# Kernel tuning notes

Hardware: AMD Instinct MI355X
Metric: run time of the kernel (lower is better)

## Reference

```python
import jax, jax.numpy as jnp
import numpy as np

N, E = 50000, 800000
F_IN, E_DIM, D, H = 128, 64, 64, 4  # per-head channels D, heads H; concat=False -> out dim D
GROUPS = 16
EPS = 1e-5


def _p(key, shape, scale):
    return (jax.random.normal(key, shape, dtype=jnp.float32) * scale)


def setup_inputs() -> dict:
    key = jax.random.key(0)
    ks = jax.random.split(key, 40)
    inp = {
        "x": jax.random.normal(ks[0], (N, F_IN), dtype=jnp.float32),
        "edge_index": jax.random.randint(ks[1], (2, E), 0, N, dtype=jnp.int64),
        "edge_attr": jax.random.normal(ks[2], (E, E_DIM), dtype=jnp.float32),
    }
    # TransformerConv params, layer i: Wq/Wk/Wv [in, H*D] (+bias), We [E_DIM, H*D] (no bias),
    # Wskip [in, D] (+bias).  Layer 1 in=F_IN, layers 2/3 in=D.
    idx = 3
    for i, fin in zip((1, 2, 3), (F_IN, D, D)):
        s = 1.0 / np.sqrt(fin)
        se = 1.0 / np.sqrt(E_DIM)
        inp[f"Wq{i}"] = _p(ks[idx + 0], (fin, H * D), s)
        inp[f"bq{i}"] = jnp.zeros((H * D,), jnp.float32)
        inp[f"Wk{i}"] = _p(ks[idx + 1], (fin, H * D), s)
        inp[f"bk{i}"] = jnp.zeros((H * D,), jnp.float32)
        inp[f"Wv{i}"] = _p(ks[idx + 2], (fin, H * D), s)
        inp[f"bv{i}"] = jnp.zeros((H * D,), jnp.float32)
        inp[f"We{i}"] = _p(ks[idx + 3], (E_DIM, H * D), se)
        inp[f"Wskip{i}"] = _p(ks[idx + 4], (fin, D), s)
        inp[f"bskip{i}"] = jnp.zeros((D,), jnp.float32)
        idx += 5
    inp["gn_w"] = jnp.ones((D,), jnp.float32)
    inp["gn_b"] = jnp.zeros((D,), jnp.float32)
    return inp


def transformer_conv(x, src, dst, edge_attr, Wq, bq, Wk, bk, Wv, bv, We, Wskip, bskip):
    n = x.shape[0]
    q = (x @ Wq + bq).reshape(n, H, D)
    k = (x @ Wk + bk).reshape(n, H, D)
    v = (x @ Wv + bv).reshape(n, H, D)
    e = (edge_attr @ We).reshape(-1, H, D)  # [E,H,D]
    k_e = k[src] + e                          # edge-level key
    v_e = v[src] + e                          # edge-level value
    alpha = jnp.einsum('ehd,ehd->eh', q[dst], k_e) / np.sqrt(D)  # [E,H]
    # segment softmax over incoming edges of each dst node
    amax = jax.ops.segment_max(alpha, dst, num_segments=n)
    amax = jnp.where(jnp.isfinite(amax), amax, 0.0)
    ex = jnp.exp(alpha - amax[dst])
    denom = jax.ops.segment_sum(ex, dst, num_segments=n)
    attn = ex / (denom[dst] + 1e-16)
    out = jax.ops.segment_sum(attn[:, :, None] * v_e, dst, num_segments=n)  # [N,H,D]
    out = out.mean(axis=1)                     # concat=False -> mean over heads
    return out + (x @ Wskip + bskip)           # root_weight skip


def group_norm(x, w, b):
    n, c = x.shape
    xg = x.reshape(n, GROUPS, c // GROUPS)
    mu = xg.mean(axis=2, keepdims=True)
    var = xg.var(axis=2, keepdims=True)
    xn = ((xg - mu) * jax.lax.rsqrt(var + EPS)).reshape(n, c)
    return xn * w + b


def reference(x, edge_index, edge_attr,
              Wq1, bq1, Wk1, bk1, Wv1, bv1, We1, Wskip1, bskip1,
              Wq2, bq2, Wk2, bk2, Wv2, bv2, We2, Wskip2, bskip2,
              Wq3, bq3, Wk3, bk3, Wv3, bv3, We3, Wskip3, bskip3,
              gn_w, gn_b):
    src, dst = edge_index[0], edge_index[1]
    layers = [
        (Wq1, bq1, Wk1, bk1, Wv1, bv1, We1, Wskip1, bskip1),
        (Wq2, bq2, Wk2, bk2, Wv2, bv2, We2, Wskip2, bskip2),
        (Wq3, bq3, Wk3, bk3, Wv3, bv3, We3, Wskip3, bskip3),
    ]
    h = x
    for prm in layers:
        h = transformer_conv(h, src, dst, edge_attr, *prm)
        h = group_norm(h, gn_w, gn_b)
        h = jax.nn.gelu(h, approximate=False)
    return h
```

## Files before the change

kernel.cpp:

```cpp
#include <hip/hip_runtime.h>
#include <math.h>

#define NN 50000
#define NE 800000
#define NCOLS 1088

typedef long long i64;
typedef unsigned short u16;
typedef short bf16x8 __attribute__((ext_vector_type(8)));
typedef unsigned short u16x8 __attribute__((ext_vector_type(8)));
typedef float f32x4 __attribute__((ext_vector_type(4)));

static __device__ __forceinline__ float bf2f(u16 u) {
  union { float f; unsigned b; } x; x.b = ((unsigned)u) << 16; return x.f;
}
static __device__ __forceinline__ u16 f2bf(float f) {
  union { float f; unsigned b; } x; x.f = f;
  unsigned r = x.b + 0x7FFFu + ((x.b >> 16) & 1u);
  return (u16)(r >> 16);
}

__global__ void detect_i64(const int* __restrict__ ei32, int* __restrict__ flag) {
  int i = blockIdx.x * blockDim.x + threadIdx.x;
  if (i < 2048) {
    if (ei32[2 * i + 1] != 0) atomicOr(flag, 1);
  }
}

__global__ void extract_edges(const void* __restrict__ ei, const int* __restrict__ flag,
                              int* __restrict__ src32, int* __restrict__ dst32, int ne) {
  int is32 = *flag;
  int i = blockIdx.x * blockDim.x + threadIdx.x;
  int st = gridDim.x * blockDim.x;
  if (is32) {
    const int* p = (const int*)ei;
    for (; i < ne; i += st) { src32[i] = p[i]; dst32[i] = p[ne + i]; }
  } else {
    const i64* p = (const i64*)ei;
    for (; i < ne; i += st) { src32[i] = (int)p[i]; dst32[i] = (int)p[ne + i]; }
  }
}

__global__ void hist_kernel(const int* __restrict__ dst, int* __restrict__ deg, int ne) {
  int i = blockIdx.x * blockDim.x + threadIdx.x;
  int st = gridDim.x * blockDim.x;
  for (; i < ne; i += st) atomicAdd(&deg[dst[i]], 1);
}

#define SCHUNK 1024
__global__ void scanA(const int* __restrict__ deg, int* __restrict__ row_ptr,
                      int* __restrict__ csum, int n) {
  __shared__ int buf[SCHUNK];
  int c = blockIdx.x, t = threadIdx.x;
  int idx = c * SCHUNK + t;
  int v = (idx < n) ? deg[idx] : 0;
  buf[t] = v;
  __syncthreads();
  for (int off = 1; off < SCHUNK; off <<= 1) {
    int x = (t >= off) ? buf[t - off] : 0;
    __syncthreads();
    buf[t] += x;
    __syncthreads();
  }
  if (idx < n) row_ptr[idx + 1] = buf[t];
  if (t == SCHUNK - 1) csum[c] = buf[t];
}

__global__ void scanB(int* __restrict__ csum, int nchunks) {
  if (threadIdx.x == 0 && blockIdx.x == 0) {
    int run = 0;
    for (int c = 0; c < nchunks; ++c) { int v = csum[c]; csum[c] = run; run += v; }
  }
}

__global__ void scanC(int* __restrict__ row_ptr, const int* __restrict__ csum, int n) {
  int c = blockIdx.x, t = threadIdx.x;
  int idx = c * SCHUNK + t;
  if (idx < n) row_ptr[idx + 1] += csum[c];
  if (idx == 0) row_ptr[0] = 0;
}

__global__ void scatter_kernel(const int* __restrict__ src, const int* __restrict__ dst,
                               const int* __restrict__ row_ptr, int* __restrict__ cursor,
                               int* __restrict__ src_sorted, int* __restrict__ eid_sorted, int ne) {
  int i = blockIdx.x * blockDim.x + threadIdx.x;
  int st = gridDim.x * blockDim.x;
  for (; i < ne; i += st) {
    int d = dst[i];
    int pos = row_ptr[d] + atomicAdd(&cursor[d], 1);
    src_sorted[pos] = src[i];
    eid_sorted[pos] = i;
  }
}

__global__ void sort_lists(const int* __restrict__ row_ptr, int* __restrict__ src_sorted,
                           int* __restrict__ eid_sorted, int n) {
  int node = blockIdx.x * blockDim.x + threadIdx.x;
  if (node >= n) return;
  int beg = row_ptr[node], end = row_ptr[node + 1];
  for (int a = beg + 1; a < end; ++a) {
    int e = eid_sorted[a], s = src_sorted[a];
    int b = a - 1;
    while (b >= beg && eid_sorted[b] > e) {
      eid_sorted[b + 1] = eid_sorted[b];
      src_sorted[b + 1] = src_sorted[b];
      --b;
    }
    eid_sorted[b + 1] = e; src_sorted[b + 1] = s;
  }
}

__global__ void ea_gather(const int* __restrict__ eid_sorted, const float* __restrict__ ea,
                          float* __restrict__ ea_csr, int ne) {
  long total = (long)ne * 16;
  long st = (long)gridDim.x * blockDim.x;
  for (long i = (long)blockIdx.x * blockDim.x + threadIdx.x; i < total; i += st) {
    int j = (int)(i >> 4);
    int c = (int)(i & 15);
    int e = eid_sorted[j];
    ((float4*)ea_csr)[i] = ((const float4*)ea)[(size_t)e * 16 + c];
  }
}

__global__ void cvt_split(const float* __restrict__ in, u16* __restrict__ hi,
                          u16* __restrict__ lo, int nElem) {
  int i = blockIdx.x * blockDim.x + threadIdx.x;
  int st = gridDim.x * blockDim.x;
  for (; i < nElem; i += st) {
    float v = in[i];
    u16 h = f2bf(v);
    hi[i] = h;
    lo[i] = f2bf(v - bf2f(h));
  }
}

__global__ void prep_wt(const float* __restrict__ Wq, const float* __restrict__ Wk,
                        const float* __restrict__ Wv, const float* __restrict__ We,
                        const float* __restrict__ Wsk, float* __restrict__ Wt, int fin) {
  int i = blockIdx.x * blockDim.x + threadIdx.x;
  if (i >= NCOLS * fin) return;
  int col = i / fin, k = i % fin;
  float val;
  if (col < 768) {
    const float* W = (col < 256) ? Wq : (col < 512) ? Wk : Wv;
    val = W[k * 256 + (col & 255)];
  } else if (col < 1024) {
    int idx = col - 768; int h = idx >> 6, ce = idx & 63;
    float a = 0.f;
    for (int d = 0; d < 64; ++d) a += Wq[k * 256 + h * 64 + d] * We[ce * 256 + h * 64 + d];
    val = a;
  } else {
    val = Wsk[k * 64 + (col - 1024)];
  }
  Wt[(size_t)col * fin + k] = val;
}

__global__ void prep_bias(const float* __restrict__ bq, const float* __restrict__ bk,
                          const float* __restrict__ bv, const float* __restrict__ We,
                          const float* __restrict__ bsk, float* __restrict__ bb) {
  int col = blockIdx.x * blockDim.x + threadIdx.x;
  if (col >= NCOLS) return;
  float val;
  if (col < 768) {
    const float* b = (col < 256) ? bq : (col < 512) ? bk : bv;
    val = b[col & 255];
  } else if (col < 1024) {
    int idx = col - 768; int h = idx >> 6, ce = idx & 63;
    float a = 0.f;
    for (int d = 0; d < 64; ++d) a += bq[h * 64 + d] * We[ce * 256 + h * 64 + d];
    val = a;
  } else {
    val = bsk[col - 1024];
  }
  bb[col] = val;
}

__global__ void prep_wpost(const float* __restrict__ We, float* __restrict__ Wt2) {
  int i = blockIdx.x * blockDim.x + threadIdx.x;
  if (i >= 64 * 256) return;
  int col = i >> 8, k = i & 255;
  int h = k >> 6, ce = k & 63;
  Wt2[i] = We[ce * 256 + h * 64 + col];
}

__global__ __launch_bounds__(256) void node_gemm_mfma(
    const u16* __restrict__ Xhi, const u16* __restrict__ Xlo,
    const u16* __restrict__ Whi, const u16* __restrict__ Wlo,
    const float* __restrict__ bb,
    float* __restrict__ qq_tab, float* __restrict__ kv_tab,
    float* __restrict__ skip_tab, int n, int fin) {
  __shared__ __align__(16) u16 Ah[64][72];
  __shared__ __align__(16) u16 Al[64][72];
  __shared__ __align__(16) u16 Bh[64][72];
  __shared__ __align__(16) u16 Bl[64][72];
  int tid = threadIdx.x, wave = tid >> 6, lane = tid & 63;
  int c0 = blockIdx.x * 64, m0 = blockIdx.y * 64;
  f32x4 acc[4];
  #pragma unroll
  for (int i = 0; i < 4; ++i) acc[i] = (f32x4){0.f, 0.f, 0.f, 0.f};

  int lr = tid >> 2, sg = (tid & 3) * 16;
  for (int k0 = 0; k0 < fin; k0 += 64) {
    u16x8 z = {0, 0, 0, 0, 0, 0, 0, 0};
    u16x8 a0 = z, a1 = z, l0 = z, l1 = z;
    if (m0 + lr < n) {
      const u16* ph = &Xhi[(size_t)(m0 + lr) * fin + k0 + sg];
      a0 = *(const u16x8*)ph; a1 = *(const u16x8*)(ph + 8);
      const u16* pl = &Xlo[(size_t)(m0 + lr) * fin + k0 + sg];
      l0 = *(const u16x8*)pl; l1 = *(const u16x8*)(pl + 8);
    }
    *(u16x8*)&Ah[lr][sg] = a0; *(u16x8*)&Ah[lr][sg + 8] = a1;
    *(u16x8*)&Al[lr][sg] = l0; *(u16x8*)&Al[lr][sg + 8] = l1;
    {
      const u16* ph = &Whi[(size_t)(c0 + lr) * fin + k0 + sg];
      *(u16x8*)&Bh[lr][sg] = *(const u16x8*)ph;
      *(u16x8*)&Bh[lr][sg + 8] = *(const u16x8*)(ph + 8);
      const u16* pl = &Wlo[(size_t)(c0 + lr) * fin + k0 + sg];
      *(u16x8*)&Bl[lr][sg] = *(const u16x8*)pl;
      *(u16x8*)&Bl[lr][sg + 8] = *(const u16x8*)(pl + 8);
    }
    __syncthreads();
    int arow = wave * 16 + (lane & 15);
    int kb = (lane >> 4) * 8;
    #pragma unroll
    for (int ks = 0; ks < 2; ++ks) {
      bf16x8 ah = *(const bf16x8*)&Ah[arow][ks * 32 + kb];
      bf16x8 al_ = *(const bf16x8*)&Al[arow][ks * 32 + kb];
      #pragma unroll
      for (int nf = 0; nf < 4; ++nf) {
        bf16x8 bh = *(const bf16x8*)&Bh[nf * 16 + (lane & 15)][ks * 32 + kb];
        bf16x8 bl = *(const bf16x8*)&Bl[nf * 16 + (lane & 15)][ks * 32 + kb];
        acc[nf] = __builtin_amdgcn_mfma_f32_16x16x32_bf16(ah, bh, acc[nf], 0, 0, 0);
        acc[nf] = __builtin_amdgcn_mfma_f32_16x16x32_bf16(ah, bl, acc[nf], 0, 0, 0);
        acc[nf] = __builtin_amdgcn_mfma_f32_16x16x32_bf16(al_, bh, acc[nf], 0, 0, 0);
      }
    }
    __syncthreads();
  }
  int rbase = m0 + wave * 16 + (lane >> 4) * 4;
  int cl = lane & 15;
  #pragma unroll
  for (int nf = 0; nf < 4; ++nf) {
    int col = c0 + nf * 16 + cl;
    float bias = bb[col];
    #pragma unroll
    for (int r = 0; r < 4; ++r) {
      int row = rbase + r;
      if (row >= n) continue;
      float val = acc[nf][r] + bias;
      if (col < 256)        qq_tab[(size_t)row * 512 + col] = val;
      else if (col < 768)   kv_tab[(size_t)row * 512 + col - 256] = val;
      else if (col < 1024)  qq_tab[(size_t)row * 512 + col - 512] = val;
      else                  skip_tab[(size_t)row * 64 + col - 1024] = val;
    }
  }
}

__global__ __launch_bounds__(256) void attn_kernel_v6(
    const int* __restrict__ row_ptr, const int* __restrict__ src_sorted,
    const int* __restrict__ eid_sorted, const float* __restrict__ ea,
    const float* __restrict__ ea_csr, int use_csr,
    const float* __restrict__ qq_tab, const float* __restrict__ kv_tab,
    float* __restrict__ avs_tab, float* __restrict__ awn_tab, int n) {
  int tid = threadIdx.x;
  int wave = tid >> 6, lane = tid & 63;
  int c16 = lane & 15;
  const float4* qq4 = (const float4*)qq_tab;
  const float4* kv4 = (const float4*)kv_tab;
  const float4* ec4 = (const float4*)ea_csr;
  const float4* e4p = (const float4*)ea;

  int node = blockIdx.x * 4 + wave;
  if (node >= n) return;
  int beg = row_ptr[node];
  int deg = row_ptr[node + 1] - beg;

  float4 q4 = qq4[(size_t)node * 128 + lane];
  float4 t4 = qq4[(size_t)node * 128 + 64 + lane];

  float m = -INFINITY, s = 0.f;
  float4 av = make_float4(0.f, 0.f, 0.f, 0.f);
  float4 aw = make_float4(0.f, 0.f, 0.f, 0.f);

#define LDE(j_, K_, V_, E_)                                   \
  {                                                           \
    int jc = (j_); int jm = beg + deg - 1;                    \
    if (jc > jm) jc = jm;                                     \
    int s_ = src_sorted[jc];                                  \
    const float4* kr = kv4 + (size_t)s_ * 128;                \
    K_ = kr[lane]; V_ = kr[64 + lane];                        \
    if (use_csr) E_ = ec4[(size_t)jc * 16 + c16];             \
    else { int e_ = eid_sorted[jc];                           \
           E_ = e4p[(size_t)e_ * 16 + c16]; }                 \
  }

#define PROC(K_, V_, E_)                                      \
  {                                                           \
    float p = q4.x * K_.x + q4.y * K_.y + q4.z * K_.z + q4.w * K_.w \
            + t4.x * E_.x + t4.y * E_.y + t4.z * E_.z + t4.w * E_.w; \
    p += __shfl_xor(p, 1);                                    \
    p += __shfl_xor(p, 2);                                    \
    p += __shfl_xor(p, 4);                                    \
    p += __shfl_xor(p, 8);                                    \
    p *= 0.125f;                                              \
    float d_ = p - m;                                         \
    float e_ = __expf(-fabsf(d_));                            \
    float sc = d_ > 0.f ? e_ : 1.f;                           \
    float pp = d_ > 0.f ? 1.f : e_;                           \
    m = fmaxf(m, p);                                          \
    s = s * sc + pp;                                          \
    av.x = av.x * sc + pp * V_.x; av.y = av.y * sc + pp * V_.y; \
    av.z = av.z * sc + pp * V_.z; av.w = av.w * sc + pp * V_.w; \
    aw.x = aw.x * sc + pp * E_.x; aw.y = aw.y * sc + pp * E_.y; \
    aw.z = aw.z * sc + pp * E_.z; aw.w = aw.w * sc + pp * E_.w; \
  }

  if (deg > 0) {
    float4 KA, VA, EA, KB, VB, EB;
    LDE(beg + 0, KA, VA, EA);
    LDE(beg + 1, KB, VB, EB);
    int t = 0;
    for (; t + 1 < deg; t += 2) {
      {
        float4 nK, nV, nE;
        LDE(beg + t + 2, nK, nV, nE);
        PROC(KA, VA, EA);
        KA = nK; VA = nV; EA = nE;
      }
      {
        float4 nK, nV, nE;
        LDE(beg + t + 3, nK, nV, nE);
        PROC(KB, VB, EB);
        KB = nK; VB = nV; EB = nE;
      }
    }
    if (t < deg) PROC(KA, VA, EA);
  }

  float inv = s > 0.f ? 1.f / s : 0.f;
  float4 awn = make_float4(aw.x * inv, aw.y * inv, aw.z * inv, aw.w * inv);
  float4 avn = make_float4(av.x * inv, av.y * inv, av.z * inv, av.w * inv);

  ((float4*)awn_tab)[(size_t)node * 64 + lane] = awn;

  avn.x += __shfl_xor(avn.x, 16); avn.y += __shfl_xor(avn.y, 16);
  avn.z += __shfl_xor(avn.z, 16); avn.w += __shfl_xor(avn.w, 16);
  avn.x += __shfl_xor(avn.x, 32); avn.y += __shfl_xor(avn.y, 32);
  avn.z += __shfl_xor(avn.z, 32); avn.w += __shfl_xor(avn.w, 32);
  if (lane < 16)
    ((float4*)avs_tab)[(size_t)node * 16 + c16] = avn;
}

__global__ __launch_bounds__(256) void post_gn(
    const float* __restrict__ A, const float* __restrict__ B,
    const float* __restrict__ avs, const float* __restrict__ skip,
    const float* __restrict__ gnw, const float* __restrict__ gnb,
    float* __restrict__ out_f32, u16* __restrict__ out_hi, u16* __restrict__ out_lo, int n) {
  __shared__ __align__(16) float Xs[128][68];
  __shared__ __align__(16) float Ws[64][68];
  int tid = threadIdx.x;
  int tx = tid & 15, ty = tid >> 4;
  int m0 = blockIdx.x * 128;
  float acc[8][4];
  #pragma unroll
  for (int i = 0; i < 8; ++i)
    #pragma unroll
    for (int j = 0; j < 4; ++j) acc[i][j] = 0.f;

  for (int k0 = 0; k0 < 256; k0 += 64) {
    #pragma unroll
    for (int p = 0; p < 8; ++p) {
      int r = ty + 16 * p;
      float4 xv = make_float4(0.f, 0.f, 0.f, 0.f);
      if (m0 + r < n) xv = *(const float4*)&A[(size_t)(m0 + r) * 256 + k0 + tx * 4];
      *(float4*)&Xs[r][tx * 4] = xv;
    }
    #pragma unroll
    for (int p = 0; p < 4; ++p) {
      int r = ty + 16 * p;
      float4 wv = *(const float4*)&B[(size_t)r * 256 + k0 + tx * 4];
      *(float4*)&Ws[r][tx * 4] = wv;
    }
    __syncthreads();
    #pragma unroll 4
    for (int kk = 0; kk < 64; kk += 4) {
      float4 a[8], b[4];
      #pragma unroll
      for (int i = 0; i < 8; ++i) a[i] = *(const float4*)&Xs[ty + 16 * i][kk];
      #pragma unroll
      for (int j = 0; j < 4; ++j) b[j] = *(const float4*)&Ws[tx + 16 * j][kk];
      #pragma unroll
      for (int i = 0; i < 8; ++i)
        #pragma unroll
        for (int j = 0; j < 4; ++j) {
          acc[i][j] = fmaf(a[i].x, b[j].x, acc[i][j]);
          acc[i][j] = fmaf(a[i].y, b[j].y, acc[i][j]);
          acc[i][j] = fmaf(a[i].z, b[j].z, acc[i][j]);
          acc[i][j] = fmaf(a[i].w, b[j].w, acc[i][j]);
        }
    }
    __syncthreads();
  }
  #pragma unroll
  for (int j = 0; j < 4; ++j)
    #pragma unroll
    for (int i = 0; i < 8; ++i)
      Xs[ty + 16 * i][tx + 16 * j] = acc[i][j];
  __syncthreads();

  #pragma unroll
  for (int rep = 0; rep < 8; ++rep) {
    int id = tid + 256 * rep;
    int rl = id >> 4, grp = id & 15;
    int row = m0 + rl;
    if (row >= n) continue;
    float4 a = ((const float4*)avs)[(size_t)row * 16 + grp];
    float4 sk = ((const float4*)skip)[(size_t)row * 16 + grp];
    float4 gw = ((const float4*)gnw)[grp];
    float4 gb = ((const float4*)gnb)[grp];
    float p0 = Xs[rl][grp * 4 + 0], p1 = Xs[rl][grp * 4 + 1];
    float p2 = Xs[rl][grp * 4 + 2], p3 = Xs[rl][grp * 4 + 3];
    float v0 = 0.25f * (a.x + p0) + sk.x;
    float v1 = 0.25f * (a.y + p1) + sk.y;
    float v2 = 0.25f * (a.z + p2) + sk.z;
    float v3 = 0.25f * (a.w + p3) + sk.w;
    float mu = ((v0 + v1) + (v2 + v3)) * 0.25f;
    float d0 = v0 - mu, d1 = v1 - mu, d2 = v2 - mu, d3 = v3 - mu;
    float var = ((d0 * d0 + d1 * d1) + (d2 * d2 + d3 * d3)) * 0.25f;
    float r = rsqrtf(var + 1e-5f);
    float y0 = d0 * r * gw.x + gb.x;
    float y1 = d1 * r * gw.y + gb.y;
    float y2 = d2 * r * gw.z + gb.z;
    float y3 = d3 * r * gw.w + gb.w;
    #define GELU(y) (0.5f * (y) * (1.0f + erff((y) * 0.70710678118654752f)))
    float g0 = GELU(y0), g1 = GELU(y1), g2 = GELU(y2), g3 = GELU(y3);
    if (out_f32) {
      float4 o; o.x = g0; o.y = g1; o.z = g2; o.w = g3;
      ((float4*)out_f32)[(size_t)row * 16 + grp] = o;
    } else {
      u16 h0 = f2bf(g0), h1 = f2bf(g1), h2 = f2bf(g2), h3 = f2bf(g3);
      ushort4 hv; hv.x = h0; hv.y = h1; hv.z = h2; hv.w = h3;
      *(ushort4*)&out_hi[(size_t)row * 64 + grp * 4] = hv;
      ushort4 lv;
      lv.x = f2bf(g0 - bf2f(h0)); lv.y = f2bf(g1 - bf2f(h1));
      lv.z = f2bf(g2 - bf2f(h2)); lv.w = f2bf(g3 - bf2f(h3));
      *(ushort4*)&out_lo[(size_t)row * 64 + grp * 4] = lv;
    }
  }
}

extern "C" void kernel_launch(void* const* d_in, const int* in_sizes, int n_in,
                              void* d_out, int out_size, void* d_ws, size_t ws_size,
                              hipStream_t stream) {
  (void)in_sizes; (void)n_in;
  const float* x = (const float*)d_in[0];
  const void* ei = d_in[1];
  const float* ea = (const float*)d_in[2];
  const float *Wq[3], *bq[3], *Wk[3], *bk[3], *Wv[3], *bv[3], *We[3], *Wsk[3], *bsk[3];
  for (int L = 0; L < 3; ++L) {
    int b = 3 + 9 * L;
    Wq[L] = (const float*)d_in[b + 0]; bq[L] = (const float*)d_in[b + 1];
    Wk[L] = (const float*)d_in[b + 2]; bk[L] = (const float*)d_in[b + 3];
    Wv[L] = (const float*)d_in[b + 4]; bv[L] = (const float*)d_in[b + 5];
    We[L] = (const float*)d_in[b + 6]; Wsk[L] = (const float*)d_in[b + 7];
    bsk[L] = (const float*)d_in[b + 8];
  }
  const float* gnw = (const float*)d_in[30];
  const float* gnb = (const float*)d_in[31];

  char* p = (char*)d_ws;
  auto alloc = [&](size_t bytes) -> void* {
    void* r = (void*)p;
    p += (bytes + 255) & ~(size_t)255;
    return r;
  };
  float* qq_tab = (float*)alloc((size_t)NN * 512 * 4);
  float* kv_tab = (float*)alloc((size_t)NN * 512 * 4);
  float* skip_tab = (float*)alloc((size_t)NN * 64 * 4);
  float* avs_tab = (float*)alloc((size_t)NN * 64 * 4);
  float* awn_tab = (float*)alloc((size_t)NN * 256 * 4);
  u16* xhi = (u16*)alloc((size_t)NN * 128 * 2);
  u16* xlo = (u16*)alloc((size_t)NN * 128 * 2);
  u16* hhi = (u16*)alloc((size_t)NN * 64 * 2);
  u16* hlo = (u16*)alloc((size_t)NN * 64 * 2);
  int* row_ptr = (int*)alloc((size_t)(NN + 1) * 4);
  int* deg = (int*)alloc((size_t)NN * 4);
  int* cursor = (int*)alloc((size_t)NN * 4);
  int* csum = (int*)alloc(1024 * 4);
  int* src_sorted = (int*)alloc((size_t)NE * 4);
  int* eid_sorted = (int*)alloc((size_t)NE * 4);
  int* src32 = (int*)alloc((size_t)NE * 4);
  int* dst32 = (int*)alloc((size_t)NE * 4);
  int* flag = (int*)alloc(256);
  float* Wt[3]; float* bb[3]; float* Wt2[3];
  u16 *whi[3], *wlo[3];
  Wt[0] = (float*)alloc((size_t)NCOLS * 128 * 4);
  Wt[1] = (float*)alloc((size_t)NCOLS * 64 * 4);
  Wt[2] = (float*)alloc((size_t)NCOLS * 64 * 4);
  whi[0] = (u16*)alloc((size_t)NCOLS * 128 * 2);
  wlo[0] = (u16*)alloc((size_t)NCOLS * 128 * 2);
  whi[1] = (u16*)alloc((size_t)NCOLS * 64 * 2);
  wlo[1] = (u16*)alloc((size_t)NCOLS * 64 * 2);
  whi[2] = (u16*)alloc((size_t)NCOLS * 64 * 2);
  wlo[2] = (u16*)alloc((size_t)NCOLS * 64 * 2);
  for (int L = 0; L < 3; ++L) bb[L] = (float*)alloc((size_t)NCOLS * 4);
  for (int L = 0; L < 3; ++L) Wt2[L] = (float*)alloc((size_t)64 * 256 * 4);

  if ((size_t)(p - (char*)d_ws) > ws_size) {
    hipMemsetAsync(d_out, 0, (size_t)out_size * 4, stream);
    return;
  }

  float* ea_csr = nullptr;
  int use_csr = 0;
  {
    size_t need = (size_t)(p - (char*)d_ws) + (size_t)NE * 64 * 4 + 256;
    if (need <= ws_size) {
      ea_csr = (float*)alloc((size_t)NE * 64 * 4);
      use_csr = 1;
    }
  }

  hipMemsetAsync(deg, 0, (size_t)NN * 4, stream);
  hipMemsetAsync(cursor, 0, (size_t)NN * 4, stream);
  hipMemsetAsync(flag, 0, 4, stream);

  detect_i64<<<8, 256, 0, stream>>>((const int*)ei, flag);
  extract_edges<<<2048, 256, 0, stream>>>(ei, flag, src32, dst32, NE);

  hist_kernel<<<2048, 256, 0, stream>>>(dst32, deg, NE);
  int nchunks = (NN + SCHUNK - 1) / SCHUNK;
  scanA<<<nchunks, SCHUNK, 0, stream>>>(deg, row_ptr, csum, NN);
  scanB<<<1, 64, 0, stream>>>(csum, nchunks);
  scanC<<<nchunks, SCHUNK, 0, stream>>>(row_ptr, csum, NN);
  scatter_kernel<<<2048, 256, 0, stream>>>(src32, dst32, row_ptr, cursor, src_sorted, eid_sorted, NE);
  sort_lists<<<(NN + 255) / 256, 256, 0, stream>>>(row_ptr, src_sorted, eid_sorted, NN);
  if (use_csr)
    ea_gather<<<2048, 256, 0, stream>>>(eid_sorted, ea, ea_csr, NE);

  cvt_split<<<2048, 256, 0, stream>>>(x, xhi, xlo, NN * 128);

  for (int L = 0; L < 3; ++L) {
    int fin = (L == 0) ? 128 : 64;
    prep_wt<<<(NCOLS * fin + 255) / 256, 256, 0, stream>>>(Wq[L], Wk[L], Wv[L], We[L], Wsk[L], Wt[L], fin);
    prep_bias<<<(NCOLS + 255) / 256, 256, 0, stream>>>(bq[L], bk[L], bv[L], We[L], bsk[L], bb[L]);
    prep_wpost<<<64, 256, 0, stream>>>(We[L], Wt2[L]);
    cvt_split<<<(NCOLS * fin + 255) / 256, 256, 0, stream>>>(Wt[L], whi[L], wlo[L], NCOLS * fin);
  }

  const u16* hi_in = xhi;
  const u16* lo_in = xlo;
  int nblk = (NN + 3) / 4;
  for (int L = 0; L < 3; ++L) {
    int fin = (L == 0) ? 128 : 64;
    dim3 g(17, (NN + 63) / 64);
    node_gemm_mfma<<<g, 256, 0, stream>>>(hi_in, lo_in, whi[L], wlo[L], bb[L],
                                          qq_tab, kv_tab, skip_tab, NN, fin);
    attn_kernel_v6<<<nblk, 256, 0, stream>>>(
        row_ptr, src_sorted, eid_sorted, ea, ea_csr, use_csr,
        qq_tab, kv_tab, avs_tab, awn_tab, NN);
    post_gn<<<(NN + 127) / 128, 256, 0, stream>>>(
        awn_tab, Wt2[L], avs_tab, skip_tab, gnw, gnb,
        (L == 2) ? (float*)d_out : nullptr,
        (L < 2) ? hhi : nullptr, (L < 2) ? hlo : nullptr, NN);
    hi_in = hhi; lo_in = hlo;
  }
}
```

Before: 1.536 ms.

## Split fused attention kernel into edge-score, softmax-value, and edge-accumulate passes

Replaces the single fused attention kernel with three kernels. The first computes the edge-attribute part of each score, the second gathers K/V, finishes the online softmax and stores per-edge alphas plus per-node max and sum, and the third re-reads the edge attributes to build the normalized weighted sum. The aim is to cut register pressure and the per-edge load width of the main gather loop. In exchange the edge attributes are read twice, there are two extra launches, and a new per-edge alpha table adds global memory traffic.

```diff
diff --git a/kernel.cpp b/kernel.cpp
--- a/kernel.cpp
+++ b/kernel.cpp
@@ -256,19 +256,43 @@
   }
 }
 
-__global__ __launch_bounds__(256) void attn_kernel_v6(
-    const int* __restrict__ row_ptr, const int* __restrict__ src_sorted,
-    const int* __restrict__ eid_sorted, const float* __restrict__ ea,
-    const float* __restrict__ ea_csr, int use_csr,
-    const float* __restrict__ qq_tab, const float* __restrict__ kv_tab,
-    float* __restrict__ avs_tab, float* __restrict__ awn_tab, int n) {
+__global__ __launch_bounds__(256) void edge_scores(
+    const int* __restrict__ row_ptr, const int* __restrict__ eid_sorted,
+    const float* __restrict__ ea, const float* __restrict__ ea_csr, int use_csr,
+    const float* __restrict__ qq_tab, float* __restrict__ al_tab, int n) {
   int tid = threadIdx.x;
   int wave = tid >> 6, lane = tid & 63;
-  int c16 = lane & 15;
+  int h = lane >> 4, c16 = lane & 15;
+  int node = blockIdx.x * 4 + wave;
+  if (node >= n) return;
+  int beg = row_ptr[node], end = row_ptr[node + 1];
+  const float4* qq4 = (const float4*)qq_tab;
+  const float4* ec4 = (const float4*)ea_csr;
+  const float4* e4p = (const float4*)ea;
+  float4 t4 = qq4[(size_t)node * 128 + 64 + lane];
+  for (int j = beg; j < end; ++j) {
+    float4 E;
+    if (use_csr) E = ec4[(size_t)j * 16 + c16];
+    else { int e_ = eid_sorted[j]; E = e4p[(size_t)e_ * 16 + c16]; }
+    float p = t4.x * E.x + t4.y * E.y + t4.z * E.z + t4.w * E.w;
+    p += __shfl_xor(p, 1);
+    p += __shfl_xor(p, 2);
+    p += __shfl_xor(p, 4);
+    p += __shfl_xor(p, 8);
+    if (c16 == 0) al_tab[(size_t)j * 4 + h] = p;
+  }
+}
+
+__global__ __launch_bounds__(256) void attn_B(
+    const int* __restrict__ row_ptr, const int* __restrict__ src_sorted,
+    const float* __restrict__ qq_tab, const float* __restrict__ kv_tab,
+    float* __restrict__ al_tab, float* __restrict__ ms_tab,
+    float* __restrict__ avs_tab, int n) {
+  int tid = threadIdx.x;
+  int wave = tid >> 6, lane = tid & 63;
+  int h = lane >> 4, c16 = lane & 15;
   const float4* qq4 = (const float4*)qq_tab;
   const float4* kv4 = (const float4*)kv_tab;
-  const float4* ec4 = (const float4*)ea_csr;
-  const float4* e4p = (const float4*)ea;
 
   int node = blockIdx.x * 4 + wave;
   if (node >= n) return;
@@ -276,72 +300,68 @@
   int deg = row_ptr[node + 1] - beg;
 
   float4 q4 = qq4[(size_t)node * 128 + lane];
-  float4 t4 = qq4[(size_t)node * 128 + 64 + lane];
-
   float m = -INFINITY, s = 0.f;
   float4 av = make_float4(0.f, 0.f, 0.f, 0.f);
-  float4 aw = make_float4(0.f, 0.f, 0.f, 0.f);
-
-#define LDE(j_, K_, V_, E_)                                   \
+
+#define LDB(j_, K_, V_, L_)                                   \
   {                                                           \
     int jc = (j_); int jm = beg + deg - 1;                    \
     if (jc > jm) jc = jm;                                     \
     int s_ = src_sorted[jc];                                  \
     const float4* kr = kv4 + (size_t)s_ * 128;                \
     K_ = kr[lane]; V_ = kr[64 + lane];                        \
-    if (use_csr) E_ = ec4[(size_t)jc * 16 + c16];             \
-    else { int e_ = eid_sorted[jc];                           \
-           E_ = e4p[(size_t)e_ * 16 + c16]; }                 \
-  }
-
-#define PROC(K_, V_, E_)                                      \
+    L_ = al_tab[(size_t)jc * 4 + h];                          \
+  }
+
+#define PROCB(j_, K_, V_, L_)                                 \
   {                                                           \
-    float p = q4.x * K_.x + q4.y * K_.y + q4.z * K_.z + q4.w * K_.w \
-            + t4.x * E_.x + t4.y * E_.y + t4.z * E_.z + t4.w * E_.w; \
+    float p = q4.x * K_.x + q4.y * K_.y + q4.z * K_.z + q4.w * K_.w; \
     p += __shfl_xor(p, 1);                                    \
     p += __shfl_xor(p, 2);                                    \
     p += __shfl_xor(p, 4);                                    \
     p += __shfl_xor(p, 8);                                    \
-    p *= 0.125f;                                              \
-    float d_ = p - m;                                         \
+    float alpha = (p + L_) * 0.125f;                          \
+    if (c16 == 0) al_tab[(size_t)(j_) * 4 + h] = alpha;       \
+    float d_ = alpha - m;                                     \
     float e_ = __expf(-fabsf(d_));                            \
     float sc = d_ > 0.f ? e_ : 1.f;                           \
     float pp = d_ > 0.f ? 1.f : e_;                           \
-    m = fmaxf(m, p);                                          \
+    m = fmaxf(m, alpha);                                      \
     s = s * sc + pp;                                          \
     av.x = av.x * sc + pp * V_.x; av.y = av.y * sc + pp * V_.y; \
     av.z = av.z * sc + pp * V_.z; av.w = av.w * sc + pp * V_.w; \
-    aw.x = aw.x * sc + pp * E_.x; aw.y = aw.y * sc + pp * E_.y; \
-    aw.z = aw.z * sc + pp * E_.z; aw.w = aw.w * sc + pp * E_.w; \
   }
 
   if (deg > 0) {
-    float4 KA, VA, EA, KB, VB, EB;
-    LDE(beg + 0, KA, VA, EA);
-    LDE(beg + 1, KB, VB, EB);
+    float4 KA, VA, KB, VB;
+    float LA, LB;
+    LDB(beg + 0, KA, VA, LA);
+    LDB(beg + 1, KB, VB, LB);
     int t = 0;
     for (; t + 1 < deg; t += 2) {
       {
-        float4 nK, nV, nE;
-        LDE(beg + t + 2, nK, nV, nE);
-        PROC(KA, VA, EA);
-        KA = nK; VA = nV; EA = nE;
+        float4 nK, nV; float nL;
+        LDB(beg + t + 2, nK, nV, nL);
+        PROCB(beg + t, KA, VA, LA);
+        KA = nK; VA = nV; LA = nL;
       }
       {
-        float4 nK, nV, nE;
-        LDE(beg + t + 3, nK, nV, nE);
-        PROC(KB, VB, EB);
-        KB = nK; VB = nV; EB = nE;
+        float4 nK, nV; float nL;
+        LDB(beg + t + 3, nK, nV, nL);
+        PROCB(beg + t + 1, KB, VB, LB);
+        KB = nK; VB = nV; LB = nL;
       }
     }
-    if (t < deg) PROC(KA, VA, EA);
+    if (t < deg) PROCB(beg + t, KA, VA, LA);
   }
 
   float inv = s > 0.f ? 1.f / s : 0.f;
-  float4 awn = make_float4(aw.x * inv, aw.y * inv, aw.z * inv, aw.w * inv);
   float4 avn = make_float4(av.x * inv, av.y * inv, av.z * inv, av.w * inv);
 
-  ((float4*)awn_tab)[(size_t)node * 64 + lane] = awn;
+  if (c16 == 0) {
+    ms_tab[(size_t)node * 8 + h * 2] = m;
+    ms_tab[(size_t)node * 8 + h * 2 + 1] = s;
+  }
 
   avn.x += __shfl_xor(avn.x, 16); avn.y += __shfl_xor(avn.y, 16);
   avn.z += __shfl_xor(avn.z, 16); avn.w += __shfl_xor(avn.w, 16);
@@ -349,6 +369,36 @@
   avn.z += __shfl_xor(avn.z, 32); avn.w += __shfl_xor(avn.w, 32);
   if (lane < 16)
     ((float4*)avs_tab)[(size_t)node * 16 + c16] = avn;
+}
+
+__global__ __launch_bounds__(256) void aw_accum(
+    const int* __restrict__ row_ptr, const int* __restrict__ eid_sorted,
+    const float* __restrict__ ea, const float* __restrict__ ea_csr, int use_csr,
+    const float* __restrict__ al_tab, const float* __restrict__ ms_tab,
+    float* __restrict__ awn_tab, int n) {
+  int tid = threadIdx.x;
+  int wave = tid >> 6, lane = tid & 63;
+  int h = lane >> 4, c16 = lane & 15;
+  int node = blockIdx.x * 4 + wave;
+  if (node >= n) return;
+  int beg = row_ptr[node], end = row_ptr[node + 1];
+  const float4* ec4 = (const float4*)ea_csr;
+  const float4* e4p = (const float4*)ea;
+  float m = ms_tab[(size_t)node * 8 + h * 2];
+  float s = ms_tab[(size_t)node * 8 + h * 2 + 1];
+  float inv = s > 0.f ? 1.f / s : 0.f;
+  float4 aw = make_float4(0.f, 0.f, 0.f, 0.f);
+  for (int j = beg; j < end; ++j) {
+    float alpha = al_tab[(size_t)j * 4 + h];
+    float4 E;
+    if (use_csr) E = ec4[(size_t)j * 16 + c16];
+    else { int e_ = eid_sorted[j]; E = e4p[(size_t)e_ * 16 + c16]; }
+    float u = __expf(alpha - m);
+    aw.x = fmaf(u, E.x, aw.x); aw.y = fmaf(u, E.y, aw.y);
+    aw.z = fmaf(u, E.z, aw.z); aw.w = fmaf(u, E.w, aw.w);
+  }
+  ((float4*)awn_tab)[(size_t)node * 64 + lane] =
+      make_float4(aw.x * inv, aw.y * inv, aw.z * inv, aw.w * inv);
 }
 
 __global__ __launch_bounds__(256) void post_gn(
@@ -479,6 +529,8 @@
   float* skip_tab = (float*)alloc((size_t)NN * 64 * 4);
   float* avs_tab = (float*)alloc((size_t)NN * 64 * 4);
   float* awn_tab = (float*)alloc((size_t)NN * 256 * 4);
+  float* al_tab = (float*)alloc((size_t)NE * 4 * 4);
+  float* ms_tab = (float*)alloc((size_t)NN * 8 * 4);
   u16* xhi = (u16*)alloc((size_t)NN * 128 * 2);
   u16* xlo = (u16*)alloc((size_t)NN * 128 * 2);
   u16* hhi = (u16*)alloc((size_t)NN * 64 * 2);
@@ -556,9 +608,12 @@
     dim3 g(17, (NN + 63) / 64);
     node_gemm_mfma<<<g, 256, 0, stream>>>(hi_in, lo_in, whi[L], wlo[L], bb[L],
                                           qq_tab, kv_tab, skip_tab, NN, fin);
-    attn_kernel_v6<<<nblk, 256, 0, stream>>>(
-        row_ptr, src_sorted, eid_sorted, ea, ea_csr, use_csr,
-        qq_tab, kv_tab, avs_tab, awn_tab, NN);
+    edge_scores<<<nblk, 256, 0, stream>>>(row_ptr, eid_sorted, ea, ea_csr, use_csr,
+                                          qq_tab, al_tab, NN);
+    attn_B<<<nblk, 256, 0, stream>>>(row_ptr, src_sorted, qq_tab, kv_tab,
+                                     al_tab, ms_tab, avs_tab, NN);
+    aw_accum<<<nblk, 256, 0, stream>>>(row_ptr, eid_sorted, ea, ea_csr, use_csr,
+                                       al_tab, ms_tab, awn_tab, NN);
     post_gn<<<(NN + 127) / 128, 256, 0, stream>>>(
         awn_tab, Wt2[L], avs_tab, skip_tab, gnw, gnb,
         (L == 2) ? (float*)d_out : nullptr,
```

Result: slower. 2.028 ms (+32.0%).
